# Performance work log

Hardware: AMD Instinct MI355X
Metric: run time of the kernel (lower is better)

## Reference

```python
import jax, jax.numpy as jnp
import numpy as np

D_MODEL = 1024
HEADS = 16
HEAD_DIM = D_MODEL // HEADS


def setup_inputs() -> dict:
    key = jax.random.key(0)
    ks = jax.random.split(key, 11)
    B, S = 2, 2048
    scale = 1.0 / np.sqrt(D_MODEL)
    inp = {
        "Q": jax.random.normal(ks[0], (B, S, D_MODEL), jnp.float32),
        "K": jax.random.normal(ks[1], (B, S, D_MODEL), jnp.float32),
        "V": jax.random.normal(ks[2], (B, S, D_MODEL), jnp.float32),
        "Wq": jax.random.normal(ks[3], (D_MODEL, D_MODEL), jnp.float32) * scale,
        "bq": jnp.zeros((D_MODEL,), jnp.float32),
        "Wk": jax.random.normal(ks[4], (D_MODEL, D_MODEL), jnp.float32) * scale,
        "bk": jnp.zeros((D_MODEL,), jnp.float32),
        "Wv": jax.random.normal(ks[5], (D_MODEL, D_MODEL), jnp.float32) * scale,
        "bv": jnp.zeros((D_MODEL,), jnp.float32),
        "Wo": jax.random.normal(ks[6], (D_MODEL, D_MODEL), jnp.float32) * scale,
        "bo": jnp.zeros((D_MODEL,), jnp.float32),
    }
    return inp


def reference(Q, K, V, Wq, bq, Wk, bk, Wv, bv, Wo, bo):
    B, S, _ = Q.shape
    # Linear projections (nn.Linear: x @ W^T + b), split into heads: [B, H, S, Dh]
    def proj(x, W, b):
        y = x @ W.T + b
        return y.reshape(B, S, HEADS, HEAD_DIM).transpose(0, 2, 1, 3)

    q = proj(Q, Wq, bq)
    k = proj(K, Wk, bk)
    v = proj(V, Wv, bv)

    # Scaled dot-product attention (dropout is identity in eval / p=0)
    scores = jnp.einsum("bhqd,bhkd->bhqk", q, k) / jnp.sqrt(
        jnp.asarray(HEAD_DIM, q.dtype)
    )
    weights = jax.nn.softmax(scores, axis=-1)
    ctx = jnp.einsum("bhqk,bhkd->bhqd", weights, v)  # [B, H, S, Dh]

    # Concatenate heads and output projection
    concat = ctx.transpose(0, 2, 1, 3).reshape(B, S, D_MODEL)
    return concat @ Wo.T + bo
```

## Files before the change

kernel.cpp:

```cpp
#include <hip/hip_runtime.h>
#include <hip/hip_bf16.h>

#define D_MODEL 1024
#define HEADS 16
#define HDIM 64
#define BATCH 2
#define SEQ 2048
#define MROWS (BATCH*SEQ)

typedef __attribute__((ext_vector_type(8))) short bf16x8;
typedef __attribute__((ext_vector_type(4))) float f32x4;
typedef __attribute__((ext_vector_type(16))) float f32x16;
typedef __attribute__((ext_vector_type(4))) float float4v;
typedef __attribute__((ext_vector_type(4))) unsigned u32x4;
typedef __attribute__((ext_vector_type(4))) short s16x4;

typedef const __attribute__((address_space(1))) void gconst_t;
typedef __attribute__((address_space(3))) void lds_t;
#define GLD16(g, l) __builtin_amdgcn_global_load_lds((gconst_t*)(g), (lds_t*)(l), 16, 0, 0)

#if __has_builtin(__builtin_amdgcn_exp2f)
#define EXP2(x) __builtin_amdgcn_exp2f(x)
#else
#define EXP2(x) __builtin_exp2f(x)
#endif

__device__ __forceinline__ unsigned short f2b(float f) {
  unsigned u = __builtin_bit_cast(unsigned, f);
  u += 0x7fffu + ((u >> 16) & 1u);
  return (unsigned short)(u >> 16);
}

__device__ __forceinline__ unsigned cvtpk(float lo, float hi) {
  unsigned r;
  asm volatile("v_cvt_pk_bf16_f32 %0, %1, %2" : "=v"(r) : "v"(lo), "v"(hi));
  return r;
}

__global__ __launch_bounds__(256)
void cast_all(const float* __restrict__ Q, const float* __restrict__ K,
              const float* __restrict__ V, const float* __restrict__ Wq,
              const float* __restrict__ Wk, const float* __restrict__ Wv,
              const float* __restrict__ Wo, char* __restrict__ ws)
{
  const size_t MB = 1024*1024;
  int b = blockIdx.x;
  const float* src; short* dst; int rb;
  if (b < 6144) {
    int t = b >> 11; rb = b & 2047;
    src = (t == 0) ? Q : (t == 1) ? K : V;
    dst = (short*)(ws + (size_t)t*8*MB);
  } else {
    int t = (b - 6144) >> 9; rb = (b - 6144) & 511;
    src = (t == 0) ? Wq : (t == 1) ? Wk : (t == 2) ? Wv : Wo;
    dst = (short*)(ws + (24 + 2*(size_t)t)*MB);
  }
  int i = rb*256 + threadIdx.x;
  const float4v* s = (const float4v*)src;
  float4v a = s[2*(size_t)i], c = s[2*(size_t)i + 1];
  bf16x8 o;
  o[0] = (short)f2b(a[0]); o[1] = (short)f2b(a[1]);
  o[2] = (short)f2b(a[2]); o[3] = (short)f2b(a[3]);
  o[4] = (short)f2b(c[0]); o[5] = (short)f2b(c[1]);
  o[6] = (short)f2b(c[2]); o[7] = (short)f2b(c[3]);
  *(bf16x8*)(dst + 8*(size_t)i) = o;
}

__global__ __launch_bounds__(256)
void gemm_qkv(const short* __restrict__ Qb, const short* __restrict__ Kb,
              const short* __restrict__ Vb, const short* __restrict__ Wqb,
              const short* __restrict__ Wkb, const short* __restrict__ Wvb,
              const float* __restrict__ bq, const float* __restrict__ bk,
              const float* __restrict__ bv, short* __restrict__ qp,
              short* __restrict__ kp, short* __restrict__ vp)
{
  __shared__ __align__(16) short smem[128*129];
  short* lA = smem;
  short* lB = smem + 128*64;
  short* lT = smem;

  const int z = blockIdx.z;
  const short* A = (z == 0) ? Qb : (z == 1) ? Kb : Vb;
  const short* W = (z == 0) ? Wqb : (z == 1) ? Wkb : Wvb;
  const float* bias = (z == 0) ? bq : (z == 1) ? bk : bv;

  const int tid  = threadIdx.x;
  const int wid  = tid >> 6;
  const int lane = tid & 63;
  const int bm = blockIdx.x, bn = blockIdx.y;
  const int wr = wid >> 1, wc = wid & 1;

  f32x4 acc[4][4] = {};

  const int srow = tid >> 3;
  const int cswz = (((tid & 7) * 16) ^ ((srow & 7) << 4)) >> 1;
  const short* gA = A + (size_t)(bm*128 + srow)*D_MODEL + cswz;
  const short* gB = W + (size_t)(bn*128 + srow)*D_MODEL + cswz;
  short* lA0 = &lA[(     wid*8)*64];
  short* lA1 = &lA[(32 + wid*8)*64];
  short* lA2 = &lA[(64 + wid*8)*64];
  short* lA3 = &lA[(96 + wid*8)*64];
  short* lB0 = &lB[(     wid*8)*64];
  short* lB1 = &lB[(32 + wid*8)*64];
  short* lB2 = &lB[(64 + wid*8)*64];
  short* lB3 = &lB[(96 + wid*8)*64];

  const int fro = lane & 15;
  const int xr7 = (fro & 7) << 4;
  const int c0  = ((((lane >> 4) << 4))      ^ xr7) >> 1;
  const int c1  = ((64 + ((lane >> 4) << 4)) ^ xr7) >> 1;

  for (int kt = 0; kt < D_MODEL/64; ++kt) {
    const int ko = kt*64;
    GLD16(gA + ko,               lA0);
    GLD16(gA + 32*D_MODEL + ko,  lA1);
    GLD16(gA + 64*D_MODEL + ko,  lA2);
    GLD16(gA + 96*D_MODEL + ko,  lA3);
    GLD16(gB + ko,               lB0);
    GLD16(gB + 32*D_MODEL + ko,  lB1);
    GLD16(gB + 64*D_MODEL + ko,  lB2);
    GLD16(gB + 96*D_MODEL + ko,  lB3);
    __syncthreads();
    #pragma unroll
    for (int ks2 = 0; ks2 < 2; ++ks2) {
      const int cc = ks2 ? c1 : c0;
      bf16x8 af[4], bfv[4];
      #pragma unroll
      for (int i = 0; i < 4; ++i)
        af[i] = *(const bf16x8*)&lA[(wr*64 + i*16 + fro)*64 + cc];
      #pragma unroll
      for (int j = 0; j < 4; ++j)
        bfv[j] = *(const bf16x8*)&lB[(wc*64 + j*16 + fro)*64 + cc];
      #pragma unroll
      for (int i = 0; i < 4; ++i)
        #pragma unroll
        for (int j = 0; j < 4; ++j)
          acc[i][j] = __builtin_amdgcn_mfma_f32_16x16x32_bf16(af[i], bfv[j], acc[i][j], 0, 0, 0);
    }
    __syncthreads();
  }

  if (z < 2) {
    const float sc = (z == 0) ? 0.125f*1.44269504f : 1.0f;
    short* out = (z == 0) ? qp : kp;
    #pragma unroll
    for (int i = 0; i < 4; ++i) {
      #pragma unroll
      for (int r = 0; r < 4; ++r) {
        const int m = bm*128 + wr*64 + i*16 + (lane>>4)*4 + r;
        const int b = m >> 11, s = m & (SEQ-1);
        #pragma unroll
        for (int j = 0; j < 4; ++j) {
          const int n = bn*128 + wc*64 + j*16 + fro;
          const int h = n >> 6, dh = n & 63;
          float v = (acc[i][j][r] + bias[n]) * sc;
          out[((size_t)(b*HEADS + h)*SEQ + s)*HDIM + dh] = (short)f2b(v);
        }
      }
    }
  } else {
    #pragma unroll
    for (int i = 0; i < 4; ++i) {
      #pragma unroll
      for (int r = 0; r < 4; ++r) {
        const int ml = wr*64 + i*16 + (lane>>4)*4 + r;
        #pragma unroll
        for (int j = 0; j < 4; ++j) {
          const int nl = wc*64 + j*16 + fro;
          lT[nl*129 + ml] = (short)f2b(acc[i][j][r] + bias[bn*128 + nl]);
        }
      }
    }
    __syncthreads();
    const int nl = tid >> 1, mh = (tid & 1) * 64;
    const int n = bn*128 + nl, h = n >> 6, dh = n & 63;
    const int b  = (bm*128) >> 11;
    const int s0 = (bm*128) & (SEQ-1);
    const size_t base = ((size_t)(b*HEADS + h)*HDIM + dh)*SEQ + s0 + mh;
    #pragma unroll
    for (int v8 = 0; v8 < 8; ++v8) {
      bf16x8 vv;
      #pragma unroll
      for (int e = 0; e < 8; ++e) vv[e] = lT[nl*129 + mh + v8*8 + e];
      *(bf16x8*)&vp[base + v8*8] = vv;
    }
  }
}

__global__ __launch_bounds__(256)
void gemm_out(const short* __restrict__ A, const short* __restrict__ W,
              const float* __restrict__ bias, float* __restrict__ out)
{
  __shared__ __align__(16) short lA[128*64];
  __shared__ __align__(16) short lB[128*64];

  const int tid  = threadIdx.x;
  const int wid  = tid >> 6;
  const int lane = tid & 63;
  const int bm = blockIdx.x, bn = blockIdx.y;
  const int wr = wid >> 1, wc = wid & 1;

  f32x4 acc[4][4] = {};
  const int srow = tid >> 3;
  const int cswz = (((tid & 7) * 16) ^ ((srow & 7) << 4)) >> 1;
  const short* gA = A + (size_t)(bm*128 + srow)*D_MODEL + cswz;
  const short* gB = W + (size_t)(bn*128 + srow)*D_MODEL + cswz;
  short* lA0 = &lA[(     wid*8)*64];
  short* lA1 = &lA[(32 + wid*8)*64];
  short* lA2 = &lA[(64 + wid*8)*64];
  short* lA3 = &lA[(96 + wid*8)*64];
  short* lB0 = &lB[(     wid*8)*64];
  short* lB1 = &lB[(32 + wid*8)*64];
  short* lB2 = &lB[(64 + wid*8)*64];
  short* lB3 = &lB[(96 + wid*8)*64];

  const int fro = lane & 15;
  const int xr7 = (fro & 7) << 4;
  const int c0  = ((((lane >> 4) << 4))      ^ xr7) >> 1;
  const int c1  = ((64 + ((lane >> 4) << 4)) ^ xr7) >> 1;

  for (int kt = 0; kt < D_MODEL/64; ++kt) {
    const int ko = kt*64;
    GLD16(gA + ko,               lA0);
    GLD16(gA + 32*D_MODEL + ko,  lA1);
    GLD16(gA + 64*D_MODEL + ko,  lA2);
    GLD16(gA + 96*D_MODEL + ko,  lA3);
    GLD16(gB + ko,               lB0);
    GLD16(gB + 32*D_MODEL + ko,  lB1);
    GLD16(gB + 64*D_MODEL + ko,  lB2);
    GLD16(gB + 96*D_MODEL + ko,  lB3);
    __syncthreads();
    #pragma unroll
    for (int ks2 = 0; ks2 < 2; ++ks2) {
      const int cc = ks2 ? c1 : c0;
      bf16x8 af[4], bfv[4];
      #pragma unroll
      for (int i = 0; i < 4; ++i)
        af[i] = *(const bf16x8*)&lA[(wr*64 + i*16 + fro)*64 + cc];
      #pragma unroll
      for (int j = 0; j < 4; ++j)
        bfv[j] = *(const bf16x8*)&lB[(wc*64 + j*16 + fro)*64 + cc];
      #pragma unroll
      for (int i = 0; i < 4; ++i)
        #pragma unroll
        for (int j = 0; j < 4; ++j)
          acc[i][j] = __builtin_amdgcn_mfma_f32_16x16x32_bf16(af[i], bfv[j], acc[i][j], 0, 0, 0);
    }
    __syncthreads();
  }

  #pragma unroll
  for (int i = 0; i < 4; ++i) {
    #pragma unroll
    for (int r = 0; r < 4; ++r) {
      const int m = bm*128 + wr*64 + i*16 + (lane>>4)*4 + r;
      #pragma unroll
      for (int j = 0; j < 4; ++j) {
        const int n = bn*128 + wc*64 + j*16 + fro;
        out[(size_t)m*D_MODEL + n] = acc[i][j][r] + bias[n];
      }
    }
  }
}

__global__ __launch_bounds__(512)
void attn(const short* __restrict__ qws, const short* __restrict__ kws,
          const short* __restrict__ vws, short* __restrict__ ctx)
{
  __shared__ __align__(16) short lK[2][2][64*64];
  __shared__ __align__(16) short lV[2][2][64*64];

  const int tid = threadIdx.x, wid = tid >> 6, lane = tid & 63;
  const int sw = wid & 3, half = wid >> 2;
  const int bid = blockIdx.x;
  const int wg = (bid & 7) * 64 + (bid >> 3);
  const int qt = wg & 15, bh = wg >> 4;
  const size_t hb = (size_t)bh * SEQ * HDIM;

  const int lane31 = lane & 31, hi = lane >> 5;
  const int tidl = sw*64 + lane;
  const int tr0  = tidl >> 3;
  const int cswz = (((tidl & 7) * 16) ^ ((tr0 & 7) << 4)) >> 1;

  const short* gK = kws + hb;
  const short* gV = vws + hb;

#define STAGEKV(t, bb) do { \
    GLD16(gK + (size_t)((t)*64 + tr0)*HDIM + cswz,      &lK[half][bb][(sw*8)*64]); \
    GLD16(gK + (size_t)((t)*64 + 32 + tr0)*HDIM + cswz, &lK[half][bb][(32+sw*8)*64]); \
    GLD16(gV + (size_t)tr0*SEQ + (t)*64 + cswz,         &lV[half][bb][(sw*8)*64]); \
    GLD16(gV + (size_t)(32+tr0)*SEQ + (t)*64 + cswz,    &lV[half][bb][(32+sw*8)*64]); \
  } while (0)

  const int kt0 = half * 16;
  STAGEKV(kt0, 0);

  const int q = qt*128 + sw*32 + lane31;
  const short* gq = qws + hb + (size_t)q*HDIM + hi*8;
  bf16x8 qf[4];
  #pragma unroll
  for (int ks = 0; ks < 4; ++ks) qf[ks] = *(const bf16x8*)(gq + ks*16);

  f32x16 o0 = {}, o1 = {};
  float lrow = 0.f;
  const int swz = (lane31 & 7) << 4;

  __syncthreads();

  for (int k2 = 0; k2 < 16; ++k2) {
    const short* Kc = &lK[half][k2 & 1][0];
    const short* Vc = &lV[half][k2 & 1][0];
    if (k2 + 1 < 16) STAGEKV(kt0 + k2 + 1, (k2 + 1) & 1);

    #pragma unroll
    for (int kb = 0; kb < 2; ++kb) {
      f32x16 s = {};
      __builtin_amdgcn_s_setprio(1);
      #pragma unroll
      for (int ks = 0; ks < 4; ++ks) {
        bf16x8 kf = *(const bf16x8*)&Kc[(kb*32 + lane31)*64 + (((ks*32 + hi*16) ^ swz) >> 1)];
        s = __builtin_amdgcn_mfma_f32_32x32x16_bf16(kf, qf[ks], s, 0, 0, 0);
      }
      __builtin_amdgcn_s_setprio(0);

      float p[16]; float rs = 0.f;
      #pragma unroll
      for (int r = 0; r < 16; ++r) { p[r] = EXP2(s[r]); rs += p[r]; }
      lrow += rs;

      unsigned w0 = cvtpk(p[0],  p[1]),  w1 = cvtpk(p[2],  p[3]);
      unsigned w2 = cvtpk(p[4],  p[5]),  w3 = cvtpk(p[6],  p[7]);
      unsigned w4 = cvtpk(p[8],  p[9]),  w5 = cvtpk(p[10], p[11]);
      unsigned w6 = cvtpk(p[12], p[13]), w7 = cvtpk(p[14], p[15]);
      unsigned y0 = hi ? w0 : w2, y1 = hi ? w1 : w3;
      unsigned y2 = hi ? w4 : w6, y3 = hi ? w5 : w7;
      unsigned z0 = (unsigned)__shfl_xor((int)y0, 32);
      unsigned z1 = (unsigned)__shfl_xor((int)y1, 32);
      unsigned z2 = (unsigned)__shfl_xor((int)y2, 32);
      unsigned z3 = (unsigned)__shfl_xor((int)y3, 32);
      u32x4 pw0 = { hi ? z0 : w0, hi ? z1 : w1, hi ? w2 : z0, hi ? w3 : z1 };
      u32x4 pw1 = { hi ? z2 : w4, hi ? z3 : w5, hi ? w6 : z2, hi ? w7 : z3 };
      bf16x8 pa0 = __builtin_bit_cast(bf16x8, pw0);
      bf16x8 pa1 = __builtin_bit_cast(bf16x8, pw1);

      __builtin_amdgcn_s_setprio(1);
      #pragma unroll
      for (int ksl = 0; ksl < 2; ++ksl) {
        const int vcol = ((kb*64 + ksl*32 + hi*16) ^ swz) >> 1;
        bf16x8 pav = ksl ? pa1 : pa0;
        bf16x8 vf0 = *(const bf16x8*)&Vc[lane31*64 + vcol];
        bf16x8 vf1 = *(const bf16x8*)&Vc[(32 + lane31)*64 + vcol];
        o0 = __builtin_amdgcn_mfma_f32_32x32x16_bf16(vf0, pav, o0, 0, 0, 0);
        o1 = __builtin_amdgcn_mfma_f32_32x32x16_bf16(vf1, pav, o1, 0, 0, 0);
      }
      __builtin_amdgcn_s_setprio(0);
    }
    __syncthreads();
  }

  lrow += __shfl_xor(lrow, 32);

  float* xo = (float*)&lK[0][0][0];
  float* xl = (float*)&lV[0][0][0];
  if (half == 1) {
    #pragma unroll
    for (int g = 0; g < 4; ++g) {
      #pragma unroll
      for (int e = 0; e < 4; ++e) {
        const int dh = g*8 + hi*4 + e;
        xo[sw*2048 + dh*32 + lane31]        = o0[g*4 + e];
        xo[sw*2048 + (32 + dh)*32 + lane31] = o1[g*4 + e];
      }
    }
    if (hi == 0) xl[sw*32 + lane31] = lrow;
  }
  __syncthreads();
  if (half == 0) {
    const float inv = 1.0f / (lrow + xl[sw*32 + lane31]);
    const int b_ = bh >> 4, h_ = bh & (HEADS-1);
    const size_t base = ((size_t)(b_*SEQ) + q)*D_MODEL + h_*HDIM;
    #pragma unroll
    for (int g = 0; g < 4; ++g) {
      s16x4 pk0, pk1;
      #pragma unroll
      for (int e = 0; e < 4; ++e) {
        const int dh = g*8 + hi*4 + e;
        pk0[e] = (short)f2b((o0[g*4+e] + xo[sw*2048 + dh*32 + lane31]) * inv);
        pk1[e] = (short)f2b((o1[g*4+e] + xo[sw*2048 + (32+dh)*32 + lane31]) * inv);
      }
      *(s16x4*)&ctx[base +      g*8 + hi*4] = pk0;
      *(s16x4*)&ctx[base + 32 + g*8 + hi*4] = pk1;
    }
  }
#undef STAGEKV
}

extern "C" void kernel_launch(void* const* d_in, const int* in_sizes, int n_in,
                              void* d_out, int out_size, void* d_ws, size_t ws_size,
                              hipStream_t stream)
{
  const float* Q  = (const float*)d_in[0];
  const float* K  = (const float*)d_in[1];
  const float* V  = (const float*)d_in[2];
  const float* Wq = (const float*)d_in[3];
  const float* bq = (const float*)d_in[4];
  const float* Wk = (const float*)d_in[5];
  const float* bk = (const float*)d_in[6];
  const float* Wv = (const float*)d_in[7];
  const float* bv = (const float*)d_in[8];
  const float* Wo = (const float*)d_in[9];
  const float* bo = (const float*)d_in[10];

  char* ws = (char*)d_ws;
  const size_t MB = 1024*1024;
  short* Qb  = (short*)(ws +  0*MB);
  short* Kb  = (short*)(ws +  8*MB);
  short* Vb  = (short*)(ws + 16*MB);
  short* Wqb = (short*)(ws + 24*MB);
  short* Wkb = (short*)(ws + 26*MB);
  short* Wvb = (short*)(ws + 28*MB);
  short* Wob = (short*)(ws + 30*MB);
  short* qp  = (short*)(ws + 32*MB);
  short* kp  = (short*)(ws + 40*MB);
  short* vp  = (short*)(ws + 48*MB);
  short* cx  = (short*)(ws + 56*MB);

  cast_all<<<8192, 256, 0, stream>>>(Q, K, V, Wq, Wk, Wv, Wo, ws);
  gemm_qkv<<<dim3(MROWS/128, D_MODEL/128, 3), 256, 0, stream>>>(
      Qb, Kb, Vb, Wqb, Wkb, Wvb, bq, bk, bv, qp, kp, vp);
  attn<<<512, 512, 0, stream>>>(qp, kp, vp, cx);
  gemm_out<<<dim3(MROWS/128, D_MODEL/128), 256, 0, stream>>>(cx, Wob, bo, (float*)d_out);
}
```

Baseline: 129.6 us.

## Double-buffer LDS tiles in QKV and output projection GEMMs

Both projection GEMMs now use two LDS buffers per operand. Each iteration issues the async global-to-LDS loads for the next K tile before computing on the current one, so memory latency overlaps MFMA work and one barrier per iteration is removed. The cost is LDS use per block doubling to 64KB, which can lower the number of resident blocks per CU.

```diff
diff --git a/kernel.cpp b/kernel.cpp
--- a/kernel.cpp
+++ b/kernel.cpp
@@ -74,10 +74,12 @@
               const float* __restrict__ bv, short* __restrict__ qp,
               short* __restrict__ kp, short* __restrict__ vp)
 {
-  __shared__ __align__(16) short smem[128*129];
-  short* lA = smem;
-  short* lB = smem + 128*64;
-  short* lT = smem;
+  __shared__ __align__(16) char smemc[65536];
+  short* const lA0 = (short*)smemc;
+  short* const lA1 = (short*)(smemc + 16384);
+  short* const lB0 = (short*)(smemc + 32768);
+  short* const lB1 = (short*)(smemc + 49152);
+  short* const lT  = (short*)smemc;
 
   const int z = blockIdx.z;
   const short* A = (z == 0) ? Qb : (z == 1) ? Kb : Vb;
@@ -96,41 +98,43 @@
   const int cswz = (((tid & 7) * 16) ^ ((srow & 7) << 4)) >> 1;
   const short* gA = A + (size_t)(bm*128 + srow)*D_MODEL + cswz;
   const short* gB = W + (size_t)(bn*128 + srow)*D_MODEL + cswz;
-  short* lA0 = &lA[(     wid*8)*64];
-  short* lA1 = &lA[(32 + wid*8)*64];
-  short* lA2 = &lA[(64 + wid*8)*64];
-  short* lA3 = &lA[(96 + wid*8)*64];
-  short* lB0 = &lB[(     wid*8)*64];
-  short* lB1 = &lB[(32 + wid*8)*64];
-  short* lB2 = &lB[(64 + wid*8)*64];
-  short* lB3 = &lB[(96 + wid*8)*64];
+
+#define QKV_STAGE(kt, bA, bB) do { \
+    const int ko_ = (kt)*64; \
+    GLD16(gA + ko_,              (bA) + (     wid*8)*64); \
+    GLD16(gA + 32*D_MODEL + ko_, (bA) + (32 + wid*8)*64); \
+    GLD16(gA + 64*D_MODEL + ko_, (bA) + (64 + wid*8)*64); \
+    GLD16(gA + 96*D_MODEL + ko_, (bA) + (96 + wid*8)*64); \
+    GLD16(gB + ko_,              (bB) + (     wid*8)*64); \
+    GLD16(gB + 32*D_MODEL + ko_, (bB) + (32 + wid*8)*64); \
+    GLD16(gB + 64*D_MODEL + ko_, (bB) + (64 + wid*8)*64); \
+    GLD16(gB + 96*D_MODEL + ko_, (bB) + (96 + wid*8)*64); \
+  } while (0)
 
   const int fro = lane & 15;
   const int xr7 = (fro & 7) << 4;
   const int c0  = ((((lane >> 4) << 4))      ^ xr7) >> 1;
   const int c1  = ((64 + ((lane >> 4) << 4)) ^ xr7) >> 1;
 
+  QKV_STAGE(0, lA0, lB0);
+  __syncthreads();
+
   for (int kt = 0; kt < D_MODEL/64; ++kt) {
-    const int ko = kt*64;
-    GLD16(gA + ko,               lA0);
-    GLD16(gA + 32*D_MODEL + ko,  lA1);
-    GLD16(gA + 64*D_MODEL + ko,  lA2);
-    GLD16(gA + 96*D_MODEL + ko,  lA3);
-    GLD16(gB + ko,               lB0);
-    GLD16(gB + 32*D_MODEL + ko,  lB1);
-    GLD16(gB + 64*D_MODEL + ko,  lB2);
-    GLD16(gB + 96*D_MODEL + ko,  lB3);
-    __syncthreads();
+    const int cur = kt & 1;
+    if (kt + 1 < D_MODEL/64)
+      QKV_STAGE(kt + 1, cur ? lA0 : lA1, cur ? lB0 : lB1);
+    const short* LA = cur ? lA1 : lA0;
+    const short* LB = cur ? lB1 : lB0;
     #pragma unroll
     for (int ks2 = 0; ks2 < 2; ++ks2) {
       const int cc = ks2 ? c1 : c0;
       bf16x8 af[4], bfv[4];
       #pragma unroll
       for (int i = 0; i < 4; ++i)
-        af[i] = *(const bf16x8*)&lA[(wr*64 + i*16 + fro)*64 + cc];
+        af[i] = *(const bf16x8*)&LA[(wr*64 + i*16 + fro)*64 + cc];
       #pragma unroll
       for (int j = 0; j < 4; ++j)
-        bfv[j] = *(const bf16x8*)&lB[(wc*64 + j*16 + fro)*64 + cc];
+        bfv[j] = *(const bf16x8*)&LB[(wc*64 + j*16 + fro)*64 + cc];
       #pragma unroll
       for (int i = 0; i < 4; ++i)
         #pragma unroll
@@ -139,6 +143,7 @@
     }
     __syncthreads();
   }
+#undef QKV_STAGE
 
   if (z < 2) {
     const float sc = (z == 0) ? 0.125f*1.44269504f : 1.0f;
@@ -191,8 +196,11 @@
 void gemm_out(const short* __restrict__ A, const short* __restrict__ W,
               const float* __restrict__ bias, float* __restrict__ out)
 {
-  __shared__ __align__(16) short lA[128*64];
-  __shared__ __align__(16) short lB[128*64];
+  __shared__ __align__(16) char smemc[65536];
+  short* const lA0 = (short*)smemc;
+  short* const lA1 = (short*)(smemc + 16384);
+  short* const lB0 = (short*)(smemc + 32768);
+  short* const lB1 = (short*)(smemc + 49152);
 
   const int tid  = threadIdx.x;
   const int wid  = tid >> 6;
@@ -205,41 +213,43 @@
   const int cswz = (((tid & 7) * 16) ^ ((srow & 7) << 4)) >> 1;
   const short* gA = A + (size_t)(bm*128 + srow)*D_MODEL + cswz;
   const short* gB = W + (size_t)(bn*128 + srow)*D_MODEL + cswz;
-  short* lA0 = &lA[(     wid*8)*64];
-  short* lA1 = &lA[(32 + wid*8)*64];
-  short* lA2 = &lA[(64 + wid*8)*64];
-  short* lA3 = &lA[(96 + wid*8)*64];
-  short* lB0 = &lB[(     wid*8)*64];
-  short* lB1 = &lB[(32 + wid*8)*64];
-  short* lB2 = &lB[(64 + wid*8)*64];
-  short* lB3 = &lB[(96 + wid*8)*64];
+
+#define OUT_STAGE(kt, bA, bB) do { \
+    const int ko_ = (kt)*64; \
+    GLD16(gA + ko_,              (bA) + (     wid*8)*64); \
+    GLD16(gA + 32*D_MODEL + ko_, (bA) + (32 + wid*8)*64); \
+    GLD16(gA + 64*D_MODEL + ko_, (bA) + (64 + wid*8)*64); \
+    GLD16(gA + 96*D_MODEL + ko_, (bA) + (96 + wid*8)*64); \
+    GLD16(gB + ko_,              (bB) + (     wid*8)*64); \
+    GLD16(gB + 32*D_MODEL + ko_, (bB) + (32 + wid*8)*64); \
+    GLD16(gB + 64*D_MODEL + ko_, (bB) + (64 + wid*8)*64); \
+    GLD16(gB + 96*D_MODEL + ko_, (bB) + (96 + wid*8)*64); \
+  } while (0)
 
   const int fro = lane & 15;
   const int xr7 = (fro & 7) << 4;
   const int c0  = ((((lane >> 4) << 4))      ^ xr7) >> 1;
   const int c1  = ((64 + ((lane >> 4) << 4)) ^ xr7) >> 1;
 
+  OUT_STAGE(0, lA0, lB0);
+  __syncthreads();
+
   for (int kt = 0; kt < D_MODEL/64; ++kt) {
-    const int ko = kt*64;
-    GLD16(gA + ko,               lA0);
-    GLD16(gA + 32*D_MODEL + ko,  lA1);
-    GLD16(gA + 64*D_MODEL + ko,  lA2);
-    GLD16(gA + 96*D_MODEL + ko,  lA3);
-    GLD16(gB + ko,               lB0);
-    GLD16(gB + 32*D_MODEL + ko,  lB1);
-    GLD16(gB + 64*D_MODEL + ko,  lB2);
-    GLD16(gB + 96*D_MODEL + ko,  lB3);
-    __syncthreads();
+    const int cur = kt & 1;
+    if (kt + 1 < D_MODEL/64)
+      OUT_STAGE(kt + 1, cur ? lA0 : lA1, cur ? lB0 : lB1);
+    const short* LA = cur ? lA1 : lA0;
+    const short* LB = cur ? lB1 : lB0;
     #pragma unroll
     for (int ks2 = 0; ks2 < 2; ++ks2) {
       const int cc = ks2 ? c1 : c0;
       bf16x8 af[4], bfv[4];
       #pragma unroll
       for (int i = 0; i < 4; ++i)
-        af[i] = *(const bf16x8*)&lA[(wr*64 + i*16 + fro)*64 + cc];
+        af[i] = *(const bf16x8*)&LA[(wr*64 + i*16 + fro)*64 + cc];
       #pragma unroll
       for (int j = 0; j < 4; ++j)
-        bfv[j] = *(const bf16x8*)&lB[(wc*64 + j*16 + fro)*64 + cc];
+        bfv[j] = *(const bf16x8*)&LB[(wc*64 + j*16 + fro)*64 + cc];
       #pragma unroll
       for (int i = 0; i < 4; ++i)
         #pragma unroll
@@ -248,6 +258,7 @@
     }
     __syncthreads();
   }
+#undef OUT_STAGE
 
   #pragma unroll
   for (int i = 0; i < 4; ++i) {
```

Measured after the change: 118.8 us. 8.4% less time.
